# Performance work log

Hardware: AMD Instinct MI355X
Metric: run time of the kernel (lower is better)

The kernel has to match this reference:

```python
import jax, jax.numpy as jnp
import numpy as np

N, E, G = 100000, 1600000, 64
FIN, D, OUT = 4, 64, 16
EPS = 1e-5


def _lin(key, fi, fo):
    kw, kb = jax.random.split(key)
    w = jax.random.normal(kw, (fi, fo), dtype=jnp.float32) / np.sqrt(fi)
    b = jnp.zeros((fo,), dtype=jnp.float32)
    return w, b


def setup_inputs() -> dict:
    key = jax.random.key(0)
    ks = jax.random.split(key, 24)
    inp = {}
    inp['h'] = jax.random.normal(ks[0], (N, FIN), dtype=jnp.float32)
    inp['pos'] = jax.random.normal(ks[1], (N, 3), dtype=jnp.float32)
    inp['edge_index'] = jax.random.randint(ks[2], (2, E), 0, N, dtype=jnp.int32)
    inp['batch'] = jnp.sort(jax.random.randint(ks[3], (N,), 0, G, dtype=jnp.int32))
    inp['fe_w'], inp['fe_b'] = _lin(ks[4], FIN, D)
    i = 5
    for c in ('c1', 'c2'):
        inp[c + 'h_w1'], inp[c + 'h_b1'] = _lin(ks[i], D, D); i += 1
        inp[c + 'h_w2'], inp[c + 'h_b2'] = _lin(ks[i], D, 3); i += 1
        inp[c + 'f_w1'], inp[c + 'f_b1'] = _lin(ks[i], D + 3, D); i += 1
        inp[c + 'f_w2'], inp[c + 'f_b2'] = _lin(ks[i], D, D); i += 1
        inp[c + 'g_w1'], inp[c + 'g_b1'] = _lin(ks[i], D, D); i += 1
        inp[c + 'g_gm'] = jnp.ones((D,), dtype=jnp.float32)
        inp[c + 'g_bt'] = jnp.zeros((D,), dtype=jnp.float32)
        inp[c + 'g_w2'], inp[c + 'g_b2'] = _lin(ks[i], D, D); i += 1
    inp['ro_w1'], inp['ro_b1'] = _lin(ks[i], D, D); i += 1
    inp['ro_w2'], inp['ro_b2'] = _lin(ks[i], D, OUT)
    return inp


def _mlp2(x, w1, b1, w2, b2):
    return jnp.maximum(x @ w1 + b1, 0.0) @ w2 + b2


def _bn(x, gm, bt):
    # BatchNorm1d in training mode: batch stats over the node axis
    m = jnp.mean(x, axis=0)
    v = jnp.var(x, axis=0)
    return (x - m) * jax.lax.rsqrt(v + EPS) * gm + bt


def _pointgnn_conv(x, pos, src, dst, hw1, hb1, hw2, hb2, fw1, fb1, fw2, fb2,
                   gw1, gb1, ggm, gbt, gw2, gb2):
    delta = _mlp2(x, hw1, hb1, hw2, hb2)                      # [N,3]
    rel = pos[src] - pos[dst] + delta[dst]                    # [E,3]
    msg = _mlp2(jnp.concatenate([rel, x[src]], axis=-1), fw1, fb1, fw2, fb2)  # [E,D]
    agg = jax.ops.segment_max(msg, dst, num_segments=x.shape[0])
    agg = jnp.where(jnp.isneginf(agg), 0.0, agg)              # empty segments -> 0
    g = jnp.maximum(agg @ gw1 + gb1, 0.0)
    g = _bn(g, ggm, gbt)
    return x + (g @ gw2 + gb2)


def reference(h, pos, edge_index, batch, fe_w, fe_b,
              c1h_w1, c1h_b1, c1h_w2, c1h_b2, c1f_w1, c1f_b1, c1f_w2, c1f_b2,
              c1g_w1, c1g_b1, c1g_gm, c1g_bt, c1g_w2, c1g_b2,
              c2h_w1, c2h_b1, c2h_w2, c2h_b2, c2f_w1, c2f_b1, c2f_w2, c2f_b2,
              c2g_w1, c2g_b1, c2g_gm, c2g_bt, c2g_w2, c2g_b2,
              ro_w1, ro_b1, ro_w2, ro_b2):
    src, dst = edge_index[0], edge_index[1]
    x = h @ fe_w + fe_b
    x = _pointgnn_conv(x, pos, src, dst, c1h_w1, c1h_b1, c1h_w2, c1h_b2,
                       c1f_w1, c1f_b1, c1f_w2, c1f_b2,
                       c1g_w1, c1g_b1, c1g_gm, c1g_bt, c1g_w2, c1g_b2)
    x = _pointgnn_conv(x, pos, src, dst, c2h_w1, c2h_b1, c2h_w2, c2h_b2,
                       c2f_w1, c2f_b1, c2f_w2, c2f_b2,
                       c2g_w1, c2g_b1, c2g_gm, c2g_bt, c2g_w2, c2g_b2)
    # global mean pool over graphs
    sums = jax.ops.segment_sum(x, batch, num_segments=G)
    cnts = jax.ops.segment_sum(jnp.ones((x.shape[0], 1), x.dtype), batch, num_segments=G)
    pooled = sums / jnp.maximum(cnts, 1.0)
    return _mlp2(pooled, ro_w1, ro_b1, ro_w2, ro_b2)
```

## Files before the change

### kernel.cpp

```cpp
#include <hip/hip_runtime.h>

#define NN 100000
#define NE 1600000
#define NG 64
#define EPS 1e-5f

#define FOR16(M) M(0) M(1) M(2) M(3) M(4) M(5) M(6) M(7) M(8) M(9) M(10) M(11) M(12) M(13) M(14) M(15)
#define WDECL(i) float4 wr##i##_;
#define LDW(i, RB, P) \
  wr##i##_.x = (P)[((RB) + 4 * i + 0) * 64 + lane]; \
  wr##i##_.y = (P)[((RB) + 4 * i + 1) * 64 + lane]; \
  wr##i##_.z = (P)[((RB) + 4 * i + 2) * 64 + lane]; \
  wr##i##_.w = (P)[((RB) + 4 * i + 3) * 64 + lane];
#define DOTR(i) { float4 v = xr[i]; \
  a0 = fmaf(v.x, wr##i##_.x, a0); a1 = fmaf(v.y, wr##i##_.y, a1); \
  a2 = fmaf(v.z, wr##i##_.z, a2); a3 = fmaf(v.w, wr##i##_.w, a3); }
#define DOTB(i, SRC) { \
  a0 = fmaf(bcast(SRC, 4 * i + 0), wr##i##_.x, a0); \
  a1 = fmaf(bcast(SRC, 4 * i + 1), wr##i##_.y, a1); \
  a2 = fmaf(bcast(SRC, 4 * i + 2), wr##i##_.z, a2); \
  a3 = fmaf(bcast(SRC, 4 * i + 3), wr##i##_.w, a3); }

__device__ __forceinline__ int wave_gid() {
  return __builtin_amdgcn_readfirstlane((int)((blockIdx.x * blockDim.x + threadIdx.x) >> 6));
}

__device__ __forceinline__ float bcast(float v, int l) {
  return __uint_as_float(__builtin_amdgcn_readlane(__float_as_uint(v), l));
}

__device__ __forceinline__ unsigned ord_of_float(float f) {
  unsigned b = __float_as_uint(f);
  return (b & 0x80000000u) ? ~b : (b | 0x80000000u);
}

__global__ void k_init_x(const float* __restrict__ h, const float* __restrict__ few,
                         const float* __restrict__ feb, float* __restrict__ x) {
  int lane = threadIdx.x & 63;
  int wg = wave_gid();
  int nw = (gridDim.x * blockDim.x) >> 6;
  float c0 = few[0 * 64 + lane], c1 = few[1 * 64 + lane];
  float c2 = few[2 * 64 + lane], c3 = few[3 * 64 + lane];
  float b = feb[lane];
  for (int n = wg; n < NN; n += nw) {
    float4 hv = *(const float4*)(h + (size_t)n * 4);
    x[(size_t)n * 64 + lane] = fmaf(hv.x, c0, fmaf(hv.y, c1, fmaf(hv.z, c2, fmaf(hv.w, c3, b))));
  }
}

__global__ void k_delta_q(const float* __restrict__ x, const float* __restrict__ pos,
                          const float* __restrict__ hw1, const float* __restrict__ hb1,
                          const float* __restrict__ hw2, const float* __restrict__ hb2,
                          float* __restrict__ q) {
  int lane = threadIdx.x & 63;
  int wg = wave_gid();
  int nw = (gridDim.x * blockDim.x) >> 6;
  FOR16(WDECL)
#define LD(i) LDW(i, 0, hw1)
  FOR16(LD)
#undef LD
  float b1 = hb1[lane];
  float u0 = hw2[lane * 3 + 0], u1 = hw2[lane * 3 + 1], u2 = hw2[lane * 3 + 2];
  float b20 = hb2[0], b21 = hb2[1], b22 = hb2[2];
  for (int n = wg; n < NN; n += nw) {
    const float4* xr = (const float4*)(x + (size_t)n * 64);
    float a0 = 0.f, a1 = 0.f, a2 = 0.f, a3 = 0.f;
    FOR16(DOTR)
    float t = fmaxf((a0 + a1) + (a2 + a3) + b1, 0.f);
    float p0 = t * u0, p1 = t * u1, p2 = t * u2;
#pragma unroll
    for (int off = 32; off; off >>= 1) {
      p0 += __shfl_xor(p0, off);
      p1 += __shfl_xor(p1, off);
      p2 += __shfl_xor(p2, off);
    }
    if (lane < 3) {
      float dc = (lane == 0) ? (p0 + b20) : ((lane == 1) ? (p1 + b21) : (p2 + b22));
      q[(size_t)n * 4 + lane] = pos[(size_t)n * 3 + lane] - dc;
    }
  }
}

__global__ void k_xa(const float* __restrict__ x, const float* __restrict__ fw1,
                     const float* __restrict__ fb1, float* __restrict__ xa,
                     unsigned* __restrict__ agg) {
  int lane = threadIdx.x & 63;
  int wg = wave_gid();
  int nw = (gridDim.x * blockDim.x) >> 6;
  FOR16(WDECL)
#define LD(i) LDW(i, 3, fw1)
  FOR16(LD)
#undef LD
  float b = fb1[lane];
  for (int n = wg; n < NN; n += nw) {
    const float4* xr = (const float4*)(x + (size_t)n * 64);
    float a0 = 0.f, a1 = 0.f, a2 = 0.f, a3 = 0.f;
    FOR16(DOTR)
    xa[(size_t)n * 64 + lane] = (a0 + a1) + (a2 + a3) + b;
    agg[(size_t)n * 64 + lane] = 0u;
  }
}

__global__ void k_edge(const float* __restrict__ xa, const float* __restrict__ pos,
                       const float* __restrict__ q, const int* __restrict__ ei,
                       const float* __restrict__ fw1, const float* __restrict__ fb2_,
                       const float* __restrict__ fw2, unsigned* __restrict__ agg) {
  int lane = threadIdx.x & 63;
  int wg = wave_gid();
  int nw = (gridDim.x * blockDim.x) >> 6;
  FOR16(WDECL)
#define LD(i) LDW(i, 0, fw2)
  FOR16(LD)
#undef LD
  float pw0 = fw1[0 * 64 + lane], pw1 = fw1[1 * 64 + lane], pw2 = fw1[2 * 64 + lane];
  float bl = fb2_[lane];
  for (int e = wg; e < NE; e += nw) {
    int src = ei[e];
    int dst = ei[NE + e];
    float4 qd = *(const float4*)(q + (size_t)dst * 4);
    float rx = pos[(size_t)src * 3 + 0] - qd.x;
    float ry = pos[(size_t)src * 3 + 1] - qd.y;
    float rz = pos[(size_t)src * 3 + 2] - qd.z;
    float hh = xa[(size_t)src * 64 + lane];
    hh = fmaxf(fmaf(rx, pw0, fmaf(ry, pw1, fmaf(rz, pw2, hh))), 0.f);
    float a0 = bl, a1 = 0.f, a2 = 0.f, a3 = 0.f;
#define DB(i) DOTB(i, hh)
    FOR16(DB)
#undef DB
    float msg = (a0 + a1) + (a2 + a3);
    unsigned u = ord_of_float(msg);
    unsigned* ap = agg + (size_t)dst * 64 + lane;
    if (u > *ap) atomicMax(ap, u);
  }
}

__global__ void k_g_bn(const unsigned* __restrict__ agg, const float* __restrict__ gw1,
                       const float* __restrict__ gb1, float* __restrict__ g,
                       float* __restrict__ bnp) {
  __shared__ float2 red[4][64];
  int lane = threadIdx.x & 63;
  int wid = threadIdx.x >> 6;
  int wg = wave_gid();
  int nw = (gridDim.x * blockDim.x) >> 6;
  FOR16(WDECL)
#define LD(i) LDW(i, 0, gw1)
  FOR16(LD)
#undef LD
  float b = gb1[lane];
  float s = 0.f, ss = 0.f;
  for (int n = wg; n < NN; n += nw) {
    unsigned u = agg[(size_t)n * 64 + lane];
    unsigned fb = (u & 0x80000000u) ? (u & 0x7fffffffu) : ~u;
    float av = (u == 0u) ? 0.f : __uint_as_float(fb);
    float a0 = 0.f, a1 = 0.f, a2 = 0.f, a3 = 0.f;
#define DB(i) DOTB(i, av)
    FOR16(DB)
#undef DB
    float gv = fmaxf((a0 + a1) + (a2 + a3) + b, 0.f);
    g[(size_t)n * 64 + lane] = gv;
    s += gv;
    ss += gv * gv;
  }
  red[wid][lane] = make_float2(s, ss);
  __syncthreads();
  if (wid == 0) {
    float2 r0 = red[0][lane], r1 = red[1][lane], r2 = red[2][lane], r3 = red[3][lane];
    bnp[(size_t)blockIdx.x * 128 + lane] = r0.x + r1.x + r2.x + r3.x;
    bnp[(size_t)blockIdx.x * 128 + 64 + lane] = r0.y + r1.y + r2.y + r3.y;
  }
}

__global__ void k_bn_final(const float* __restrict__ bnp, const float* __restrict__ gm,
                           const float* __restrict__ bt, const float* __restrict__ gw2,
                           const float* __restrict__ gb2, float* __restrict__ w2p,
                           float* __restrict__ b2p, int nblk) {
  __shared__ float sums[128];
  __shared__ float sc[64], sh[64];
  int t = threadIdx.x;
  int c = t & 63;
  int kind = t >> 6;
  float acc = 0.f;
  for (int bId = 0; bId < nblk; ++bId) acc += bnp[(size_t)bId * 128 + kind * 64 + c];
  sums[t] = acc;
  __syncthreads();
  if (t < 64) {
    float mean = sums[t] * (1.f / (float)NN);
    float var = sums[64 + t] * (1.f / (float)NN) - mean * mean;
    float scale = gm[t] * rsqrtf(var + EPS);
    sc[t] = scale;
    sh[t] = bt[t] - mean * scale;
  }
  __syncthreads();
  for (int i = t; i < 4096; i += 128) {
    int d = i >> 6;
    w2p[i] = sc[d] * gw2[i];
  }
  if (t < 64) {
    float acc2 = gb2[t];
    for (int d = 0; d < 64; ++d) acc2 = fmaf(sh[d], gw2[d * 64 + t], acc2);
    b2p[t] = acc2;
  }
}

__global__ void k_update(const float* __restrict__ g, const float* __restrict__ w2p,
                         const float* __restrict__ b2p, float* __restrict__ x) {
  int lane = threadIdx.x & 63;
  int wg = wave_gid();
  int nw = (gridDim.x * blockDim.x) >> 6;
  FOR16(WDECL)
#define LD(i) LDW(i, 0, w2p)
  FOR16(LD)
#undef LD
  float b = b2p[lane];
  for (int n = wg; n < NN; n += nw) {
    const float4* xr = (const float4*)(g + (size_t)n * 64);
    float a0 = 0.f, a1 = 0.f, a2 = 0.f, a3 = 0.f;
    FOR16(DOTR)
    size_t idx = (size_t)n * 64 + lane;
    x[idx] = x[idx] + (a0 + a1) + (a2 + a3) + b;
  }
}

__global__ void k_pool(const float* __restrict__ x, const int* __restrict__ batch,
                       float* __restrict__ pooled) {
  __shared__ float red[8][64];
  int lane = threadIdx.x & 63;
  int wid = threadIdx.x >> 6;
  int g = blockIdx.x;
  int a = 0, b = NN;
  while (a < b) {
    int m = (a + b) >> 1;
    if (batch[m] < g) a = m + 1; else b = m;
  }
  int s = a;
  b = NN;
  while (a < b) {
    int m = (a + b) >> 1;
    if (batch[m] < g + 1) a = m + 1; else b = m;
  }
  int e = a;
  float acc = 0.f;
  for (int n = s + wid; n < e; n += 8) acc += x[(size_t)n * 64 + lane];
  red[wid][lane] = acc;
  __syncthreads();
  if (wid == 0) {
    float t = 0.f;
#pragma unroll
    for (int w = 0; w < 8; ++w) t += red[w][lane];
    float cnt = (float)(e - s);
    pooled[(size_t)g * 64 + lane] = t / fmaxf(cnt, 1.f);
  }
}

__global__ void k_readout(const float* __restrict__ pooled, const float* __restrict__ w1,
                          const float* __restrict__ b1, const float* __restrict__ w2,
                          const float* __restrict__ b2, float* __restrict__ out) {
  __shared__ float hs[64];
  int lane = threadIdx.x;
  int g = blockIdx.x;
  FOR16(WDECL)
#define LD(i) LDW(i, 0, w1)
  FOR16(LD)
#undef LD
  const float4* xr = (const float4*)(pooled + (size_t)g * 64);
  float a0 = 0.f, a1 = 0.f, a2 = 0.f, a3 = 0.f;
  FOR16(DOTR)
  hs[lane] = fmaxf((a0 + a1) + (a2 + a3) + b1[lane], 0.f);
  __syncthreads();
  if (lane < 16) {
    float acc = b2[lane];
#pragma unroll
    for (int l = 0; l < 64; ++l) acc = fmaf(hs[l], w2[l * 16 + lane], acc);
    out[(size_t)g * 16 + lane] = acc;
  }
}

extern "C" void kernel_launch(void* const* d_in, const int* in_sizes, int n_in,
                              void* d_out, int out_size, void* d_ws, size_t ws_size,
                              hipStream_t stream) {
  const float* h = (const float*)d_in[0];
  const float* pos = (const float*)d_in[1];
  const int* ei = (const int*)d_in[2];
  const int* batch = (const int*)d_in[3];
  const float* fe_w = (const float*)d_in[4];
  const float* fe_b = (const float*)d_in[5];
  const float* ro_w1 = (const float*)d_in[34];
  const float* ro_b1 = (const float*)d_in[35];
  const float* ro_w2 = (const float*)d_in[36];
  const float* ro_b2 = (const float*)d_in[37];
  float* out = (float*)d_out;

  char* ws = (char*)d_ws;
  const size_t SZ_ROW = (size_t)NN * 64 * sizeof(float);
  float* x = (float*)(ws); ws += SZ_ROW;
  float* xa = (float*)(ws); ws += SZ_ROW;
  unsigned* agg = (unsigned*)(ws); ws += SZ_ROW;
  float* q = (float*)(ws); ws += (size_t)NN * 4 * sizeof(float);
  const int NBLK_BN = 256;
  float* bnp = (float*)(ws); ws += (size_t)NBLK_BN * 128 * sizeof(float);
  float* w2p = (float*)(ws); ws += 4096 * sizeof(float);
  float* b2p = (float*)(ws); ws += 256;
  float* pooled = (float*)(ws); ws += 4096 * sizeof(float);

  const int NB_NODE = 512;
  const int NB_EDGE = 4096;

  k_init_x<<<NB_NODE, 256, 0, stream>>>(h, fe_w, fe_b, x);

  for (int layer = 0; layer < 2; ++layer) {
    int base = (layer == 0) ? 6 : 20;
    const float* hw1 = (const float*)d_in[base + 0];
    const float* hb1 = (const float*)d_in[base + 1];
    const float* hw2 = (const float*)d_in[base + 2];
    const float* hb2 = (const float*)d_in[base + 3];
    const float* fw1 = (const float*)d_in[base + 4];
    const float* fb1 = (const float*)d_in[base + 5];
    const float* fw2 = (const float*)d_in[base + 6];
    const float* fb2 = (const float*)d_in[base + 7];
    const float* gw1 = (const float*)d_in[base + 8];
    const float* gb1 = (const float*)d_in[base + 9];
    const float* ggm = (const float*)d_in[base + 10];
    const float* gbt = (const float*)d_in[base + 11];
    const float* gw2 = (const float*)d_in[base + 12];
    const float* gb2 = (const float*)d_in[base + 13];

    k_delta_q<<<NB_NODE, 256, 0, stream>>>(x, pos, hw1, hb1, hw2, hb2, q);
    k_xa<<<NB_NODE, 256, 0, stream>>>(x, fw1, fb1, xa, agg);
    k_edge<<<NB_EDGE, 256, 0, stream>>>(xa, pos, q, ei, fw1, fb2, fw2, agg);
    float* g = xa;
    k_g_bn<<<NBLK_BN, 256, 0, stream>>>(agg, gw1, gb1, g, bnp);
    k_bn_final<<<1, 128, 0, stream>>>(bnp, ggm, gbt, gw2, gb2, w2p, b2p, NBLK_BN);
    k_update<<<NB_NODE, 256, 0, stream>>>(g, w2p, b2p, x);
  }

  k_pool<<<NG, 512, 0, stream>>>(x, batch, pooled);
  k_readout<<<NG, 64, 0, stream>>>(pooled, ro_w1, ro_b1, ro_w2, ro_b2, out);
}
```

Measured before the change: 1.586 ms.

## Build CSR by destination and aggregate edge max per node without atomics

Builds a destination-sorted CSR (histogram, three-pass scan, scatter) each call, then runs the edge MLP per destination node and keeps a register running max, removing per-edge atomicMax on ordered uints and the agg zeroing. It also fuses the delta and xa node projections into one kernel, pins weight registers with inline asm, and splits pooling into partial blocks that use atomicAdd with the mean scale folded into readout. The CSR build adds several kernel launches and extra atomics up front, and one wave per destination can be unbalanced across nodes with different in-degrees.

```diff
diff --git a/kernel.cpp b/kernel.cpp
--- a/kernel.cpp
+++ b/kernel.cpp
@@ -4,14 +4,17 @@
 #define NE 1600000
 #define NG 64
 #define EPS 1e-5f
+#define SCAN_NB 98
 
 #define FOR16(M) M(0) M(1) M(2) M(3) M(4) M(5) M(6) M(7) M(8) M(9) M(10) M(11) M(12) M(13) M(14) M(15)
+
 #define WDECL(i) float4 wr##i##_;
 #define LDW(i, RB, P) \
   wr##i##_.x = (P)[((RB) + 4 * i + 0) * 64 + lane]; \
   wr##i##_.y = (P)[((RB) + 4 * i + 1) * 64 + lane]; \
   wr##i##_.z = (P)[((RB) + 4 * i + 2) * 64 + lane]; \
   wr##i##_.w = (P)[((RB) + 4 * i + 3) * 64 + lane];
+#define WPIN(i) asm volatile("" : "+v"(wr##i##_.x), "+v"(wr##i##_.y), "+v"(wr##i##_.z), "+v"(wr##i##_.w));
 #define DOTR(i) { float4 v = xr[i]; \
   a0 = fmaf(v.x, wr##i##_.x, a0); a1 = fmaf(v.y, wr##i##_.y, a1); \
   a2 = fmaf(v.z, wr##i##_.z, a2); a3 = fmaf(v.w, wr##i##_.w, a3); }
@@ -21,6 +24,17 @@
   a2 = fmaf(bcast(SRC, 4 * i + 2), wr##i##_.z, a2); \
   a3 = fmaf(bcast(SRC, 4 * i + 3), wr##i##_.w, a3); }
 
+#define BDECL(i) float4 br##i##_;
+#define LDB(i, RB, P) \
+  br##i##_.x = (P)[((RB) + 4 * i + 0) * 64 + lane]; \
+  br##i##_.y = (P)[((RB) + 4 * i + 1) * 64 + lane]; \
+  br##i##_.z = (P)[((RB) + 4 * i + 2) * 64 + lane]; \
+  br##i##_.w = (P)[((RB) + 4 * i + 3) * 64 + lane];
+#define BPIN(i) asm volatile("" : "+v"(br##i##_.x), "+v"(br##i##_.y), "+v"(br##i##_.z), "+v"(br##i##_.w));
+#define DOTRB(i) { float4 v = xr[i]; \
+  a0 = fmaf(v.x, br##i##_.x, a0); a1 = fmaf(v.y, br##i##_.y, a1); \
+  a2 = fmaf(v.z, br##i##_.z, a2); a3 = fmaf(v.w, br##i##_.w, a3); }
+
 __device__ __forceinline__ int wave_gid() {
   return __builtin_amdgcn_readfirstlane((int)((blockIdx.x * blockDim.x + threadIdx.x) >> 6));
 }
@@ -29,13 +43,95 @@
   return __uint_as_float(__builtin_amdgcn_readlane(__float_as_uint(v), l));
 }
 
-__device__ __forceinline__ unsigned ord_of_float(float f) {
-  unsigned b = __float_as_uint(f);
-  return (b & 0x80000000u) ? ~b : (b | 0x80000000u);
-}
-
-__global__ void k_init_x(const float* __restrict__ h, const float* __restrict__ few,
-                         const float* __restrict__ feb, float* __restrict__ x) {
+__device__ __forceinline__ void graph_range(const int* __restrict__ batch, int g, int& s, int& e) {
+  int a = 0, b = NN;
+  while (a < b) { int m = (a + b) >> 1; if (batch[m] < g) a = m + 1; else b = m; }
+  s = a;
+  b = NN;
+  while (a < b) { int m = (a + b) >> 1; if (batch[m] < g + 1) a = m + 1; else b = m; }
+  e = a;
+}
+
+__global__ void k_zero(unsigned* __restrict__ hist, float* __restrict__ psum) {
+  int i = blockIdx.x * blockDim.x + threadIdx.x;
+  int st = gridDim.x * blockDim.x;
+  for (int j = i; j < NN; j += st) hist[j] = 0u;
+  for (int j = i; j < NG * 64; j += st) psum[j] = 0.f;
+}
+
+__global__ void k_hist(const int* __restrict__ ei, unsigned* __restrict__ hist) {
+  int i = blockIdx.x * blockDim.x + threadIdx.x;
+  int st = gridDim.x * blockDim.x;
+  for (int e = i; e < NE; e += st) atomicAdd(&hist[ei[NE + e]], 1u);
+}
+
+__global__ void k_scan1(const unsigned* __restrict__ hist, unsigned* __restrict__ coff,
+                        unsigned* __restrict__ bsum) {
+  __shared__ unsigned sd[256];
+  int t = threadIdx.x;
+  int base = blockIdx.x * 1024 + t * 4;
+  unsigned v0 = (base + 0 < NN) ? hist[base + 0] : 0u;
+  unsigned v1 = (base + 1 < NN) ? hist[base + 1] : 0u;
+  unsigned v2 = (base + 2 < NN) ? hist[base + 2] : 0u;
+  unsigned v3 = (base + 3 < NN) ? hist[base + 3] : 0u;
+  unsigned tsum = v0 + v1 + v2 + v3;
+  sd[t] = tsum;
+  __syncthreads();
+  for (int off = 1; off < 256; off <<= 1) {
+    unsigned add = (t >= off) ? sd[t - off] : 0u;
+    __syncthreads();
+    sd[t] += add;
+    __syncthreads();
+  }
+  unsigned p = sd[t] - tsum;
+  if (t == 255) bsum[blockIdx.x] = sd[255];
+  if (base + 0 < NN) coff[base + 0] = p; p += v0;
+  if (base + 1 < NN) coff[base + 1] = p; p += v1;
+  if (base + 2 < NN) coff[base + 2] = p; p += v2;
+  if (base + 3 < NN) coff[base + 3] = p;
+}
+
+__global__ void k_scan2(unsigned* __restrict__ bsum) {
+  __shared__ unsigned sd[128];
+  int t = threadIdx.x;
+  unsigned v = (t < SCAN_NB) ? bsum[t] : 0u;
+  sd[t] = v;
+  __syncthreads();
+  for (int off = 1; off < 128; off <<= 1) {
+    unsigned add = (t >= off) ? sd[t - off] : 0u;
+    __syncthreads();
+    sd[t] += add;
+    __syncthreads();
+  }
+  if (t < SCAN_NB) bsum[t] = sd[t] - v;
+}
+
+__global__ void k_scan3(unsigned* __restrict__ coff, const unsigned* __restrict__ bsum,
+                        unsigned* __restrict__ cursor) {
+  int i = blockIdx.x * blockDim.x + threadIdx.x;
+  if (i < NN) {
+    unsigned v = coff[i] + bsum[i >> 10];
+    coff[i] = v;
+    cursor[i] = v;
+  }
+  if (i == 0) coff[NN] = NE;
+}
+
+__global__ void k_scatter(const int* __restrict__ ei, unsigned* __restrict__ cursor,
+                          int* __restrict__ csrc) {
+  int i = blockIdx.x * blockDim.x + threadIdx.x;
+  int st = gridDim.x * blockDim.x;
+  for (int e = i; e < NE; e += st) {
+    int dst = ei[NE + e];
+    unsigned p = atomicAdd(&cursor[dst], 1u);
+    csrc[p] = ei[e];
+  }
+}
+
+__global__ void __launch_bounds__(256) k_init_x(const float* __restrict__ h,
+                                                const float* __restrict__ few,
+                                                const float* __restrict__ feb,
+                                                float* __restrict__ x) {
   int lane = threadIdx.x & 63;
   int wg = wave_gid();
   int nw = (gridDim.x * blockDim.x) >> 6;
@@ -48,18 +144,27 @@
   }
 }
 
-__global__ void k_delta_q(const float* __restrict__ x, const float* __restrict__ pos,
-                          const float* __restrict__ hw1, const float* __restrict__ hb1,
-                          const float* __restrict__ hw2, const float* __restrict__ hb2,
-                          float* __restrict__ q) {
+__global__ void __launch_bounds__(256) k_node_pre(
+    const float* __restrict__ x, const float* __restrict__ pos,
+    const float* __restrict__ hw1, const float* __restrict__ hb1,
+    const float* __restrict__ hw2, const float* __restrict__ hb2,
+    const float* __restrict__ fw1, const float* __restrict__ fb1,
+    float* __restrict__ q, float* __restrict__ xa) {
   int lane = threadIdx.x & 63;
   int wg = wave_gid();
   int nw = (gridDim.x * blockDim.x) >> 6;
   FOR16(WDECL)
+  FOR16(BDECL)
 #define LD(i) LDW(i, 0, hw1)
   FOR16(LD)
 #undef LD
+#define LD(i) LDB(i, 3, fw1)
+  FOR16(LD)
+#undef LD
+  FOR16(WPIN)
+  FOR16(BPIN)
   float b1 = hb1[lane];
+  float fb = fb1[lane];
   float u0 = hw2[lane * 3 + 0], u1 = hw2[lane * 3 + 1], u2 = hw2[lane * 3 + 2];
   float b20 = hb2[0], b21 = hb2[1], b22 = hb2[2];
   for (int n = wg; n < NN; n += nw) {
@@ -74,6 +179,9 @@
       p1 += __shfl_xor(p1, off);
       p2 += __shfl_xor(p2, off);
     }
+    a0 = 0.f; a1 = 0.f; a2 = 0.f; a3 = 0.f;
+    FOR16(DOTRB)
+    xa[(size_t)n * 64 + lane] = (a0 + a1) + (a2 + a3) + fb;
     if (lane < 3) {
       float dc = (lane == 0) ? (p0 + b20) : ((lane == 1) ? (p1 + b21) : (p2 + b22));
       q[(size_t)n * 4 + lane] = pos[(size_t)n * 3 + lane] - dc;
@@ -81,30 +189,12 @@
   }
 }
 
-__global__ void k_xa(const float* __restrict__ x, const float* __restrict__ fw1,
-                     const float* __restrict__ fb1, float* __restrict__ xa,
-                     unsigned* __restrict__ agg) {
-  int lane = threadIdx.x & 63;
-  int wg = wave_gid();
-  int nw = (gridDim.x * blockDim.x) >> 6;
-  FOR16(WDECL)
-#define LD(i) LDW(i, 3, fw1)
-  FOR16(LD)
-#undef LD
-  float b = fb1[lane];
-  for (int n = wg; n < NN; n += nw) {
-    const float4* xr = (const float4*)(x + (size_t)n * 64);
-    float a0 = 0.f, a1 = 0.f, a2 = 0.f, a3 = 0.f;
-    FOR16(DOTR)
-    xa[(size_t)n * 64 + lane] = (a0 + a1) + (a2 + a3) + b;
-    agg[(size_t)n * 64 + lane] = 0u;
-  }
-}
-
-__global__ void k_edge(const float* __restrict__ xa, const float* __restrict__ pos,
-                       const float* __restrict__ q, const int* __restrict__ ei,
-                       const float* __restrict__ fw1, const float* __restrict__ fb2_,
-                       const float* __restrict__ fw2, unsigned* __restrict__ agg) {
+__global__ void __launch_bounds__(256) k_edge_csr(
+    const float* __restrict__ xa, const float* __restrict__ pos,
+    const float* __restrict__ q, const unsigned* __restrict__ coff,
+    const int* __restrict__ csrc, const float* __restrict__ fw1,
+    const float* __restrict__ fb2_, const float* __restrict__ fw2,
+    float* __restrict__ agg) {
   int lane = threadIdx.x & 63;
   int wg = wave_gid();
   int nw = (gridDim.x * blockDim.x) >> 6;
@@ -112,31 +202,45 @@
 #define LD(i) LDW(i, 0, fw2)
   FOR16(LD)
 #undef LD
+  FOR16(WPIN)
   float pw0 = fw1[0 * 64 + lane], pw1 = fw1[1 * 64 + lane], pw2 = fw1[2 * 64 + lane];
   float bl = fb2_[lane];
-  for (int e = wg; e < NE; e += nw) {
-    int src = ei[e];
-    int dst = ei[NE + e];
+  const float NEGINF = __int_as_float(0xff800000);
+  for (int dst = wg; dst < NN; dst += nw) {
+    unsigned s = coff[dst], e = coff[dst + 1];
     float4 qd = *(const float4*)(q + (size_t)dst * 4);
-    float rx = pos[(size_t)src * 3 + 0] - qd.x;
-    float ry = pos[(size_t)src * 3 + 1] - qd.y;
-    float rz = pos[(size_t)src * 3 + 2] - qd.z;
-    float hh = xa[(size_t)src * 64 + lane];
-    hh = fmaxf(fmaf(rx, pw0, fmaf(ry, pw1, fmaf(rz, pw2, hh))), 0.f);
-    float a0 = bl, a1 = 0.f, a2 = 0.f, a3 = 0.f;
-#define DB(i) DOTB(i, hh)
-    FOR16(DB)
+    float mx = NEGINF;
+    if (e > s) {
+      int src = csrc[s];
+      float px = pos[(size_t)src * 3 + 0];
+      float py = pos[(size_t)src * 3 + 1];
+      float pz = pos[(size_t)src * 3 + 2];
+      float hh = xa[(size_t)src * 64 + lane];
+      for (unsigned i = s; i < e; ++i) {
+        float cpx = px, cpy = py, cpz = pz, chh = hh;
+        if (i + 1 < e) {
+          int ns = csrc[i + 1];
+          px = pos[(size_t)ns * 3 + 0];
+          py = pos[(size_t)ns * 3 + 1];
+          pz = pos[(size_t)ns * 3 + 2];
+          hh = xa[(size_t)ns * 64 + lane];
+        }
+        float rx = cpx - qd.x, ry = cpy - qd.y, rz = cpz - qd.z;
+        float pre = fmaxf(fmaf(rx, pw0, fmaf(ry, pw1, fmaf(rz, pw2, chh))), 0.f);
+        float a0 = bl, a1 = 0.f, a2 = 0.f, a3 = 0.f;
+#define DB(i) DOTB(i, pre)
+        FOR16(DB)
 #undef DB
-    float msg = (a0 + a1) + (a2 + a3);
-    unsigned u = ord_of_float(msg);
-    unsigned* ap = agg + (size_t)dst * 64 + lane;
-    if (u > *ap) atomicMax(ap, u);
-  }
-}
-
-__global__ void k_g_bn(const unsigned* __restrict__ agg, const float* __restrict__ gw1,
-                       const float* __restrict__ gb1, float* __restrict__ g,
-                       float* __restrict__ bnp) {
+        mx = fmaxf(mx, (a0 + a1) + (a2 + a3));
+      }
+    }
+    agg[(size_t)dst * 64 + lane] = (e > s) ? mx : 0.f;
+  }
+}
+
+__global__ void __launch_bounds__(256) k_g_bn(
+    const float* __restrict__ agg, const float* __restrict__ gw1,
+    const float* __restrict__ gb1, float* __restrict__ g, float* __restrict__ bnp) {
   __shared__ float2 red[4][64];
   int lane = threadIdx.x & 63;
   int wid = threadIdx.x >> 6;
@@ -146,12 +250,11 @@
 #define LD(i) LDW(i, 0, gw1)
   FOR16(LD)
 #undef LD
+  FOR16(WPIN)
   float b = gb1[lane];
   float s = 0.f, ss = 0.f;
   for (int n = wg; n < NN; n += nw) {
-    unsigned u = agg[(size_t)n * 64 + lane];
-    unsigned fb = (u & 0x80000000u) ? (u & 0x7fffffffu) : ~u;
-    float av = (u == 0u) ? 0.f : __uint_as_float(fb);
+    float av = agg[(size_t)n * 64 + lane];
     float a0 = 0.f, a1 = 0.f, a2 = 0.f, a3 = 0.f;
 #define DB(i) DOTB(i, av)
     FOR16(DB)
@@ -170,17 +273,19 @@
   }
 }
 
+#define NBLK_BN 256
 __global__ void k_bn_final(const float* __restrict__ bnp, const float* __restrict__ gm,
                            const float* __restrict__ bt, const float* __restrict__ gw2,
                            const float* __restrict__ gb2, float* __restrict__ w2p,
-                           float* __restrict__ b2p, int nblk) {
+                           float* __restrict__ b2p) {
   __shared__ float sums[128];
   __shared__ float sc[64], sh[64];
   int t = threadIdx.x;
   int c = t & 63;
   int kind = t >> 6;
   float acc = 0.f;
-  for (int bId = 0; bId < nblk; ++bId) acc += bnp[(size_t)bId * 128 + kind * 64 + c];
+#pragma unroll 8
+  for (int bId = 0; bId < NBLK_BN; ++bId) acc += bnp[(size_t)bId * 128 + kind * 64 + c];
   sums[t] = acc;
   __syncthreads();
   if (t < 64) {
@@ -197,13 +302,15 @@
   }
   if (t < 64) {
     float acc2 = gb2[t];
+#pragma unroll 8
     for (int d = 0; d < 64; ++d) acc2 = fmaf(sh[d], gw2[d * 64 + t], acc2);
     b2p[t] = acc2;
   }
 }
 
-__global__ void k_update(const float* __restrict__ g, const float* __restrict__ w2p,
-                         const float* __restrict__ b2p, float* __restrict__ x) {
+__global__ void __launch_bounds__(256) k_update(
+    const float* __restrict__ g, const float* __restrict__ w2p,
+    const float* __restrict__ b2p, float* __restrict__ x) {
   int lane = threadIdx.x & 63;
   int wg = wave_gid();
   int nw = (gridDim.x * blockDim.x) >> 6;
@@ -211,6 +318,7 @@
 #define LD(i) LDW(i, 0, w2p)
   FOR16(LD)
 #undef LD
+  FOR16(WPIN)
   float b = b2p[lane];
   for (int n = wg; n < NN; n += nw) {
     const float4* xr = (const float4*)(g + (size_t)n * 64);
@@ -221,51 +329,47 @@
   }
 }
 
-__global__ void k_pool(const float* __restrict__ x, const int* __restrict__ batch,
-                       float* __restrict__ pooled) {
+__global__ void __launch_bounds__(512) k_pool_partial(const float* __restrict__ x,
+                                                      const int* __restrict__ batch,
+                                                      float* __restrict__ psum) {
   __shared__ float red[8][64];
   int lane = threadIdx.x & 63;
   int wid = threadIdx.x >> 6;
-  int g = blockIdx.x;
-  int a = 0, b = NN;
-  while (a < b) {
-    int m = (a + b) >> 1;
-    if (batch[m] < g) a = m + 1; else b = m;
-  }
-  int s = a;
-  b = NN;
-  while (a < b) {
-    int m = (a + b) >> 1;
-    if (batch[m] < g + 1) a = m + 1; else b = m;
-  }
-  int e = a;
+  int g = blockIdx.x >> 2;
+  int part = blockIdx.x & 3;
+  int s, e;
+  graph_range(batch, g, s, e);
   float acc = 0.f;
-  for (int n = s + wid; n < e; n += 8) acc += x[(size_t)n * 64 + lane];
+  for (int n = s + part * 8 + wid; n < e; n += 32) acc += x[(size_t)n * 64 + lane];
   red[wid][lane] = acc;
   __syncthreads();
   if (wid == 0) {
-    float t = 0.f;
+    float t = acc;
 #pragma unroll
-    for (int w = 0; w < 8; ++w) t += red[w][lane];
-    float cnt = (float)(e - s);
-    pooled[(size_t)g * 64 + lane] = t / fmaxf(cnt, 1.f);
-  }
-}
-
-__global__ void k_readout(const float* __restrict__ pooled, const float* __restrict__ w1,
-                          const float* __restrict__ b1, const float* __restrict__ w2,
-                          const float* __restrict__ b2, float* __restrict__ out) {
+    for (int w = 1; w < 8; ++w) t += red[w][lane];
+    atomicAdd(&psum[(size_t)g * 64 + lane], t);
+  }
+}
+
+__global__ void __launch_bounds__(64) k_readout(
+    const float* __restrict__ psum, const int* __restrict__ batch,
+    const float* __restrict__ w1, const float* __restrict__ b1,
+    const float* __restrict__ w2, const float* __restrict__ b2,
+    float* __restrict__ out) {
   __shared__ float hs[64];
   int lane = threadIdx.x;
   int g = blockIdx.x;
+  int s, e;
+  graph_range(batch, g, s, e);
+  float scale = 1.f / fmaxf((float)(e - s), 1.f);
   FOR16(WDECL)
 #define LD(i) LDW(i, 0, w1)
   FOR16(LD)
 #undef LD
-  const float4* xr = (const float4*)(pooled + (size_t)g * 64);
+  const float4* xr = (const float4*)(psum + (size_t)g * 64);
   float a0 = 0.f, a1 = 0.f, a2 = 0.f, a3 = 0.f;
   FOR16(DOTR)
-  hs[lane] = fmaxf((a0 + a1) + (a2 + a3) + b1[lane], 0.f);
+  hs[lane] = fmaxf(((a0 + a1) + (a2 + a3)) * scale + b1[lane], 0.f);
   __syncthreads();
   if (lane < 16) {
     float acc = b2[lane];
@@ -294,16 +398,26 @@
   const size_t SZ_ROW = (size_t)NN * 64 * sizeof(float);
   float* x = (float*)(ws); ws += SZ_ROW;
   float* xa = (float*)(ws); ws += SZ_ROW;
-  unsigned* agg = (unsigned*)(ws); ws += SZ_ROW;
+  float* agg = (float*)(ws); ws += SZ_ROW;
   float* q = (float*)(ws); ws += (size_t)NN * 4 * sizeof(float);
-  const int NBLK_BN = 256;
   float* bnp = (float*)(ws); ws += (size_t)NBLK_BN * 128 * sizeof(float);
   float* w2p = (float*)(ws); ws += 4096 * sizeof(float);
   float* b2p = (float*)(ws); ws += 256;
-  float* pooled = (float*)(ws); ws += 4096 * sizeof(float);
+  float* psum = (float*)(ws); ws += (size_t)NG * 64 * sizeof(float);
+  unsigned* cursor = (unsigned*)(ws); ws += ((size_t)NN * 4 + 256);
+  unsigned* coff = (unsigned*)(ws); ws += ((size_t)(NN + 1) * 4 + 252);
+  unsigned* bsum = (unsigned*)(ws); ws += 512;
+  int* csrc = (int*)(ws); ws += (size_t)NE * 4;
 
   const int NB_NODE = 512;
   const int NB_EDGE = 4096;
+
+  k_zero<<<256, 256, 0, stream>>>(cursor, psum);
+  k_hist<<<1024, 256, 0, stream>>>(ei, cursor);
+  k_scan1<<<SCAN_NB, 256, 0, stream>>>(cursor, coff, bsum);
+  k_scan2<<<1, 128, 0, stream>>>(bsum);
+  k_scan3<<<392, 256, 0, stream>>>(coff, bsum, cursor);
+  k_scatter<<<1024, 256, 0, stream>>>(ei, cursor, csrc);
 
   k_init_x<<<NB_NODE, 256, 0, stream>>>(h, fe_w, fe_b, x);
 
@@ -324,15 +438,14 @@
     const float* gw2 = (const float*)d_in[base + 12];
     const float* gb2 = (const float*)d_in[base + 13];
 
-    k_delta_q<<<NB_NODE, 256, 0, stream>>>(x, pos, hw1, hb1, hw2, hb2, q);
-    k_xa<<<NB_NODE, 256, 0, stream>>>(x, fw1, fb1, xa, agg);
-    k_edge<<<NB_EDGE, 256, 0, stream>>>(xa, pos, q, ei, fw1, fb2, fw2, agg);
+    k_node_pre<<<NB_NODE, 256, 0, stream>>>(x, pos, hw1, hb1, hw2, hb2, fw1, fb1, q, xa);
+    k_edge_csr<<<NB_EDGE, 256, 0, stream>>>(xa, pos, q, coff, csrc, fw1, fb2, fw2, agg);
     float* g = xa;
     k_g_bn<<<NBLK_BN, 256, 0, stream>>>(agg, gw1, gb1, g, bnp);
-    k_bn_final<<<1, 128, 0, stream>>>(bnp, ggm, gbt, gw2, gb2, w2p, b2p, NBLK_BN);
+    k_bn_final<<<1, 128, 0, stream>>>(bnp, ggm, gbt, gw2, gb2, w2p, b2p);
     k_update<<<NB_NODE, 256, 0, stream>>>(g, w2p, b2p, x);
   }
 
-  k_pool<<<NG, 512, 0, stream>>>(x, batch, pooled);
-  k_readout<<<NG, 64, 0, stream>>>(pooled, ro_w1, ro_b1, ro_w2, ro_b2, out);
-}
+  k_pool_partial<<<NG * 4, 512, 0, stream>>>(x, batch, psum);
+  k_readout<<<NG, 64, 0, stream>>>(psum, batch, ro_w1, ro_b1, ro_w2, ro_b2, out);
+}
```

Measured after the change: 1.373 ms. 13.4% less time.
